# Optimization experiments

Measured on AMD Instinct MI355X. Metric: run time of the kernel, lower is better.

The kernel has to match this reference:

```python
import jax, jax.numpy as jnp
import numpy as np

D_AU, D_LM, D_GZ = 35, 196, 2   # au = 235 - 196 - 2 - 2
D, H = 128, 4
HD = D // H
LN_EPS = 1e-5


def setup_inputs() -> dict:
    key = jax.random.key(0)
    ks = jax.random.split(key, 12)
    s = lambda k, shape: jax.random.normal(k, shape, jnp.float32) * 0.02
    return {
        "video_feat": jax.random.normal(ks[0], (32, 4096, 235), jnp.float32),
        "au_w": s(ks[1], (D, D_AU)), "au_b": jnp.zeros((D,), jnp.float32),
        "lm_w": s(ks[2], (D, D_LM)), "lm_b": jnp.zeros((D,), jnp.float32),
        "gz_w": s(ks[3], (D, D_GZ)), "gz_b": jnp.zeros((D,), jnp.float32),
        "in_w": s(ks[4], (3 * D, D)), "in_b": jnp.zeros((3 * D,), jnp.float32),
        "out_w": s(ks[5], (D, D)), "out_b": jnp.zeros((D,), jnp.float32),
        "ln_g": jnp.ones((D,), jnp.float32), "ln_b": jnp.zeros((D,), jnp.float32),
        "w_w": s(ks[6], (1, D)), "w_b": jnp.zeros((1,), jnp.float32),
    }


def reference(video_feat, au_w, au_b, lm_w, lm_b, gz_w, gz_b,
              in_w, in_b, out_w, out_b, ln_g, ln_b, w_w, w_b):
    B, N, _ = video_feat.shape
    # split OpenFace3 features into semantic groups (meta dims unused, as in torch)
    au = video_feat[..., :D_AU]
    lm = video_feat[..., D_AU:D_AU + D_LM]
    gz = video_feat[..., D_AU + D_LM:D_AU + D_LM + D_GZ]
    au_h = au @ au_w.T + au_b
    lm_h = lm @ lm_w.T + lm_b
    gz_h = gz @ gz_w.T + gz_b
    tok = jnp.stack([au_h, lm_h, gz_h], axis=2).reshape(B * N, 3, D)  # (BN,3,D)

    # nn.MultiheadAttention (batch_first): packed in_proj then out_proj
    qkv = tok @ in_w.T + in_b                      # (BN,3,3D)
    q, k, v = jnp.split(qkv, 3, axis=-1)
    def heads(x):
        return x.reshape(-1, 3, H, HD).transpose(0, 2, 1, 3)  # (BN,H,3,HD)
    q, k, v = heads(q), heads(k), heads(v)
    scores = jnp.einsum('bhqd,bhkd->bhqk', q, k) / jnp.sqrt(jnp.float32(HD))
    attn = jax.nn.softmax(scores, axis=-1)
    o = jnp.einsum('bhqk,bhkd->bhqd', attn, v)
    o = o.transpose(0, 2, 1, 3).reshape(-1, 3, D)
    attn_out = o @ out_w.T + out_b

    # residual + LayerNorm
    x = attn_out + tok
    mu = x.mean(axis=-1, keepdims=True)
    var = x.var(axis=-1, keepdims=True)
    x = (x - mu) * jax.lax.rsqrt(var + LN_EPS) * ln_g + ln_b

    # softmax-weighted pooling over the 3 group tokens
    w = jax.nn.softmax((x @ w_w.T + w_b)[..., 0], axis=-1)  # (BN,3)
    fused = jnp.einsum('bt,btd->bd', w, x)
    return fused.reshape(B, N, D)
```

## Files before the change

### kernel.cpp

```cpp
#include <hip/hip_runtime.h>
#include <hip/hip_bf16.h>

typedef __hip_bfloat16 bf16;
typedef short  frag_t __attribute__((ext_vector_type(8)));
typedef float  f4     __attribute__((ext_vector_type(4)));
typedef unsigned short us8 __attribute__((ext_vector_type(8)));

#define NPOS (32 * 4096)
#define CIN  235

#define W1F 0
#define W2F 98304
#define W3F 147456
#define FRAG_TOTAL 163840
#define FP32_OFF_BYTES (FRAG_TOTAL * 2)
#define F_BIAS 0
#define F_INB  384
#define F_OUTB 768
#define F_LNG  896
#define F_LNB  1024
#define F_GW   1152
#define F_BW   1280
#define F_SGW  1281
#define WS2_BYTES (FP32_OFF_BYTES + 1282 * 4)

__device__ __forceinline__ float b2f(bf16 x) { return __bfloat162float(x); }
__device__ __forceinline__ unsigned short f2b(float v) {
    bf16 h = __float2bfloat16(v);
    return __builtin_bit_cast(unsigned short, h);
}
__device__ __forceinline__ float b2fr(unsigned short u) {
    return __bfloat162float(__builtin_bit_cast(bf16, u));
}
__device__ __forceinline__ bool probe_is_f32(const void* ln_g) {
    return *(const unsigned int*)ln_g == 0x3F800000u;
}
__device__ __forceinline__ float ldany(const void* p, int i, bool f32) {
    return f32 ? ((const float*)p)[i] : b2f(((const bf16*)p)[i]);
}
template<typename IT> __device__ __forceinline__ float ldv(const void* p, size_t i);
template<> __device__ __forceinline__ float ldv<float>(const void* p, size_t i) { return ((const float*)p)[i]; }
template<> __device__ __forceinline__ float ldv<bf16>(const void* p, size_t i)  { return b2f(((const bf16*)p)[i]); }
template<typename IT> __device__ __forceinline__ void stv(void* p, size_t i, float v);
template<> __device__ __forceinline__ void stv<float>(void* p, size_t i, float v) { ((float*)p)[i] = v; }
template<> __device__ __forceinline__ void stv<bf16>(void* p, size_t i, float v)  { ((bf16*)p)[i] = __float2bfloat16(v); }

__global__ __launch_bounds__(256) void kprep(
    const void* __restrict__ au_w, const void* __restrict__ au_b,
    const void* __restrict__ lm_w, const void* __restrict__ lm_b,
    const void* __restrict__ gz_w, const void* __restrict__ gz_b,
    const void* __restrict__ in_w, const void* __restrict__ in_b,
    const void* __restrict__ out_w, const void* __restrict__ out_b,
    const void* __restrict__ ln_g, const void* __restrict__ ln_b,
    const void* __restrict__ w_w, void* __restrict__ ws)
{
    const bool f32 = probe_is_f32(ln_g);
    int idx = blockIdx.x * 256 + threadIdx.x;
    unsigned short* wf = (unsigned short*)ws;
    float* wsf = (float*)((char*)ws + FP32_OFF_BYTES);

    if (idx < FRAG_TOTAL) {
        float val = 0.f;
        if (idx < W2F) {
            int r = idx, j = r & 7, lane = (r >> 3) & 63, q = r >> 9;
            int tn = q % 24, ks = q / 24;
            int k = ks * 32 + (lane >> 4) * 8 + j;
            int c = tn * 16 + (lane & 15);
            int t = c >> 7, jo = c & 127;
            if (t == 0 && k < 35)                   val = ldany(au_w, jo * 35 + k, f32);
            else if (t == 1 && k >= 35 && k < 231)  val = ldany(lm_w, jo * 196 + (k - 35), f32);
            else if (t == 2 && k >= 231 && k < 233) val = ldany(gz_w, jo * 2 + (k - 231), f32);
        } else if (idx < W3F) {
            int r = idx - W2F, j = r & 7, lane = (r >> 3) & 63, q = r >> 9;
            int tn = q % 24, ks = q / 24;
            int k = ks * 32 + (lane >> 4) * 8 + j;
            int c = tn * 16 + (lane & 15);
            val = ldany(in_w, c * 128 + k, f32);
        } else {
            int r = idx - W3F, j = r & 7, lane = (r >> 3) & 63, q = r >> 9;
            int tn = q & 7, ks = q >> 3;
            int k = ks * 32 + (lane >> 4) * 8 + j;
            int c = tn * 16 + (lane & 15);
            val = ldany(out_w, c * 128 + k, f32);
        }
        wf[idx] = f2b(val);
    } else if (idx < FRAG_TOTAL + 1280) {
        int i2 = idx - FRAG_TOTAL;
        float v;
        if (i2 < 384) {
            int t = i2 >> 7, jo = i2 & 127;
            const void* b = (t == 0) ? au_b : ((t == 1) ? lm_b : gz_b);
            v = ldany(b, jo, f32);
        } else if (i2 < 768)  v = ldany(in_b,  i2 - 384, f32);
        else if   (i2 < 896)  v = ldany(out_b, i2 - 768, f32);
        else if   (i2 < 1024) v = ldany(ln_g,  i2 - 896, f32);
        else if   (i2 < 1152) v = ldany(ln_b,  i2 - 1024, f32);
        else                  v = ldany(ln_g, i2 - 1152, f32) * ldany(w_w, i2 - 1152, f32);
        wsf[i2] = v;
    }
}

__global__ __launch_bounds__(64) void kscal(
    const void* __restrict__ ln_g, const void* __restrict__ ln_b,
    const void* __restrict__ w_w, const void* __restrict__ w_b,
    void* __restrict__ ws)
{
    const bool f32 = probe_is_f32(ln_g);
    float* wsf = (float*)((char*)ws + FP32_OFF_BYTES);
    int lane = threadIdx.x;
    float bw = 0.f, sg = 0.f;
    for (int j = lane; j < 128; j += 64) {
        float wwj = ldany(w_w, j, f32);
        bw += ldany(ln_b, j, f32) * wwj;
        sg += ldany(ln_g, j, f32) * wwj;
    }
#pragma unroll
    for (int off = 32; off >= 1; off >>= 1) {
        bw += __shfl_down(bw, off);
        sg += __shfl_down(sg, off);
    }
    if (lane == 0) {
        wsf[F_BW]  = bw + ldany(w_b, 0, f32);
        wsf[F_SGW] = sg;
    }
}

__global__ __launch_bounds__(256, 3) void sga_mfma(
    const void* __restrict__ vf, const void* __restrict__ ln_g,
    const void* __restrict__ ws, void* __restrict__ out)
{
    const bool f32 = probe_is_f32(ln_g);
    const int tid = threadIdx.x;
    const int w = tid >> 6, lane = tid & 63, quad = lane >> 4, l16 = lane & 15;
    const int p0 = blockIdx.x * 16;

    const frag_t* wfr = (const frag_t*)ws;
    const float*  wsf = (const float*)((const char*)ws + FP32_OFF_BYTES);

    __shared__ __align__(16) unsigned char u_buf[37632];
    __shared__ __align__(16) unsigned short s_tok[48][136];
    __shared__ float s_ar[576];
    __shared__ float s_mu[48], s_rs[48], s_w[16][3];

    unsigned short (*s_vf)[264]  = (unsigned short(*)[264])u_buf;
    unsigned short (*s_qkv)[392] = (unsigned short(*)[392])u_buf;
    float          (*s_x)[132]   = (float(*)[132])u_buf;

    for (int it = 0; it < 16; ++it) {
        int idx = it * 256 + tid;
        int row = idx >> 8, c = idx & 255;
        float v = 0.f;
        if (c < 233) {
            int gi = (p0 + row) * CIN + c;
            v = f32 ? ldv<float>(vf, gi) : ldv<bf16>(vf, gi);
        }
        s_vf[row][c] = f2b(v);
    }
    __syncthreads();

    {
        frag_t a[8];
#pragma unroll
        for (int ks = 0; ks < 8; ++ks)
            a[ks] = *(const frag_t*)&s_vf[l16][ks * 32 + quad * 8];
#pragma unroll
        for (int tn6 = 0; tn6 < 6; ++tn6) {
            int tn = w * 6 + tn6;
            f4 acc = {0.f, 0.f, 0.f, 0.f};
#pragma unroll
            for (int ks = 0; ks < 8; ++ks) {
                frag_t b = wfr[W1F / 8 + (ks * 24 + tn) * 64 + lane];
                acc = __builtin_amdgcn_mfma_f32_16x16x32_bf16(a[ks], b, acc, 0, 0, 0);
            }
            int c = tn * 16 + l16, t = c >> 7, jo = c & 127;
            float bias = wsf[F_BIAS + c];
#pragma unroll
            for (int r = 0; r < 4; ++r)
                s_tok[(quad * 4 + r) * 3 + t][jo] = f2b(acc[r] + bias);
        }
    }
    __syncthreads();

    {
        frag_t a[3][4];
#pragma unroll
        for (int rt = 0; rt < 3; ++rt)
#pragma unroll
            for (int ks = 0; ks < 4; ++ks)
                a[rt][ks] = *(const frag_t*)&s_tok[rt * 16 + l16][ks * 32 + quad * 8];
#pragma unroll
        for (int tn6 = 0; tn6 < 6; ++tn6) {
            int tn = w * 6 + tn6;
            f4 acc[3];
#pragma unroll
            for (int rt = 0; rt < 3; ++rt) acc[rt] = (f4){0.f, 0.f, 0.f, 0.f};
#pragma unroll
            for (int ks = 0; ks < 4; ++ks) {
                frag_t b = wfr[W2F / 8 + (ks * 24 + tn) * 64 + lane];
#pragma unroll
                for (int rt = 0; rt < 3; ++rt)
                    acc[rt] = __builtin_amdgcn_mfma_f32_16x16x32_bf16(a[rt][ks], b, acc[rt], 0, 0, 0);
            }
            int c = tn * 16 + l16;
            float bias = wsf[F_INB + c];
#pragma unroll
            for (int rt = 0; rt < 3; ++rt)
#pragma unroll
                for (int r = 0; r < 4; ++r)
                    s_qkv[rt * 16 + quad * 4 + r][c] = f2b(acc[rt][r] + bias);
        }
    }
    __syncthreads();

    if (tid < 192) {
        int p = tid / 12, r = tid % 12, h = r / 3, t = r % 3;
        const unsigned short* qrow = &s_qkv[p * 3 + t][h * 32];
        float sc0 = 0.f, sc1 = 0.f, sc2 = 0.f;
#pragma unroll
        for (int c4 = 0; c4 < 4; ++c4) {
            us8 qq = *(const us8*)&qrow[c4 * 8];
            float qf[8];
#pragma unroll
            for (int j = 0; j < 8; ++j) qf[j] = b2fr(qq[j]);
            us8 k0 = *(const us8*)&s_qkv[p * 3 + 0][128 + h * 32 + c4 * 8];
            us8 k1 = *(const us8*)&s_qkv[p * 3 + 1][128 + h * 32 + c4 * 8];
            us8 k2 = *(const us8*)&s_qkv[p * 3 + 2][128 + h * 32 + c4 * 8];
#pragma unroll
            for (int j = 0; j < 8; ++j) {
                sc0 += qf[j] * b2fr(k0[j]);
                sc1 += qf[j] * b2fr(k1[j]);
                sc2 += qf[j] * b2fr(k2[j]);
            }
        }
        const float scale = 0.17677669529663687f;
        sc0 *= scale; sc1 *= scale; sc2 *= scale;
        float m = fmaxf(sc0, fmaxf(sc1, sc2));
        float e0 = __expf(sc0 - m), e1 = __expf(sc1 - m), e2 = __expf(sc2 - m);
        float inv = 1.f / (e0 + e1 + e2);
        int base = ((p * 4 + h) * 3 + t) * 3;
        s_ar[base + 0] = e0 * inv;
        s_ar[base + 1] = e1 * inv;
        s_ar[base + 2] = e2 * inv;
    }
    __syncthreads();

    for (int u = 0; u < 3; ++u) {
        int unit = u * 256 + tid;
        int row = unit >> 4, c8 = (unit & 15) << 3;
        int p = row / 3, t = row - p * 3, h = c8 >> 5;
        int base = ((p * 4 + h) * 3 + t) * 3;
        float a0 = s_ar[base], a1 = s_ar[base + 1], a2 = s_ar[base + 2];
        us8 v0 = *(const us8*)&s_qkv[p * 3 + 0][256 + c8];
        us8 v1 = *(const us8*)&s_qkv[p * 3 + 1][256 + c8];
        us8 v2 = *(const us8*)&s_qkv[p * 3 + 2][256 + c8];
        us8 o;
#pragma unroll
        for (int jj = 0; jj < 8; ++jj)
            o[jj] = f2b(a0 * b2fr(v0[jj]) + a1 * b2fr(v1[jj]) + a2 * b2fr(v2[jj]));
        *(us8*)&s_qkv[row][c8] = o;
    }
    __syncthreads();

    frag_t of[3][4];
#pragma unroll
    for (int rt = 0; rt < 3; ++rt)
#pragma unroll
        for (int ks = 0; ks < 4; ++ks)
            of[rt][ks] = *(const frag_t*)&s_qkv[rt * 16 + l16][ks * 32 + quad * 8];
    __syncthreads();

    {
#pragma unroll
        for (int tn2 = 0; tn2 < 2; ++tn2) {
            int tn = w * 2 + tn2;
            f4 acc[3];
#pragma unroll
            for (int rt = 0; rt < 3; ++rt) acc[rt] = (f4){0.f, 0.f, 0.f, 0.f};
#pragma unroll
            for (int ks = 0; ks < 4; ++ks) {
                frag_t b = wfr[W3F / 8 + (ks * 8 + tn) * 64 + lane];
#pragma unroll
                for (int rt = 0; rt < 3; ++rt)
                    acc[rt] = __builtin_amdgcn_mfma_f32_16x16x32_bf16(of[rt][ks], b, acc[rt], 0, 0, 0);
            }
            int c = tn * 16 + l16;
            float ob = wsf[F_OUTB + c];
#pragma unroll
            for (int rt = 0; rt < 3; ++rt)
#pragma unroll
                for (int r = 0; r < 4; ++r) {
                    int row = rt * 16 + quad * 4 + r;
                    s_x[row][c] = acc[rt][r] + ob + b2fr(s_tok[row][c]);
                }
        }
    }
    __syncthreads();

    if (tid < 192) {
        int row = tid >> 2, part = tid & 3;
        float s = 0.f, ss = 0.f, sg = 0.f;
#pragma unroll
        for (int cc = 0; cc < 8; ++cc) {
            float4 xv = *(const float4*)&s_x[row][part * 32 + cc * 4];
            int cg = F_GW + part * 32 + cc * 4;
            s  += xv.x + xv.y + xv.z + xv.w;
            ss += xv.x * xv.x + xv.y * xv.y + xv.z * xv.z + xv.w * xv.w;
            sg += xv.x * wsf[cg] + xv.y * wsf[cg + 1] + xv.z * wsf[cg + 2] + xv.w * wsf[cg + 3];
        }
        int b = (row * 4 + part) * 3;
        s_ar[b] = s; s_ar[b + 1] = ss; s_ar[b + 2] = sg;
    }
    __syncthreads();
    if (tid < 64) {
        float lg = 0.f;
        if (lane < 48) {
            float s = 0.f, ss = 0.f, sg = 0.f;
#pragma unroll
            for (int part = 0; part < 4; ++part) {
                int b = (lane * 4 + part) * 3;
                s += s_ar[b]; ss += s_ar[b + 1]; sg += s_ar[b + 2];
            }
            float mu  = s * (1.f / 128.f);
            float var = ss * (1.f / 128.f) - mu * mu;
            float rs  = rsqrtf(var + 1e-5f);
            s_mu[lane] = mu; s_rs[lane] = rs;
            lg = wsf[F_BW] + rs * (sg - mu * wsf[F_SGW]);
        }
        float l0 = __shfl(lg, 3 * lane);
        float l1 = __shfl(lg, 3 * lane + 1);
        float l2 = __shfl(lg, 3 * lane + 2);
        if (lane < 16) {
            float m = fmaxf(l0, fmaxf(l1, l2));
            float e0 = __expf(l0 - m), e1 = __expf(l1 - m), e2 = __expf(l2 - m);
            float inv = 1.f / (e0 + e1 + e2);
            s_w[lane][0] = e0 * inv; s_w[lane][1] = e1 * inv; s_w[lane][2] = e2 * inv;
        }
    }
    __syncthreads();

    {
        int j = tid & 127;
        float g = wsf[F_LNG + j], b = wsf[F_LNB + j];
#pragma unroll
        for (int it = 0; it < 8; ++it) {
            int p = it * 2 + (tid >> 7);
            float f = 0.f;
#pragma unroll
            for (int t = 0; t < 3; ++t) {
                int row = p * 3 + t;
                f += s_w[p][t] * ((s_x[row][j] - s_mu[row]) * s_rs[row] * g + b);
            }
            size_t oidx = (size_t)(p0 + p) * 128 + j;
            if (f32) stv<float>(out, oidx, f); else stv<bf16>(out, oidx, f);
        }
    }
}

#define P 4
struct SmemFB {
    float vf[P][233];
    alignas(16) float tok[P][128][4];
    float qkv[P][3][384];
    float att[P][4][3][3];
    alignas(16) float o[P][128][4];
    float x[P][3][128];
    float red[P][3][2];
    float w[P][4];
};

template<typename IT>
__device__ void sga_fb_body(SmemFB& s,
    const void* vf, const void* au_w, const void* au_b, const void* lm_w,
    const void* lm_b, const void* gz_w, const void* gz_b, const void* in_w,
    const void* in_b, const void* out_w, const void* out_b, const void* ln_g,
    const void* ln_b, const void* w_w, const void* w_b, void* out)
{
    const int j = threadIdx.x;
    const int p0 = blockIdx.x * P;
    for (int p = 0; p < P; ++p) {
        size_t rb = (size_t)(p0 + p) * CIN;
        for (int d = j; d < 233; d += 128) s.vf[p][d] = ldv<IT>(vf, rb + d);
    }
    __syncthreads();
    {
        float a_au[P], a_lm[P], a_gz[P];
        const float bau = ldv<IT>(au_b, j), blm = ldv<IT>(lm_b, j), bgz = ldv<IT>(gz_b, j);
#pragma unroll
        for (int p = 0; p < P; ++p) { a_au[p] = bau; a_lm[p] = blm; a_gz[p] = bgz; }
        for (int d = 0; d < 35; ++d) {
            float w = ldv<IT>(au_w, j * 35 + d);
#pragma unroll
            for (int p = 0; p < P; ++p) a_au[p] += s.vf[p][d] * w;
        }
        for (int d = 0; d < 196; ++d) {
            float w = ldv<IT>(lm_w, j * 196 + d);
#pragma unroll
            for (int p = 0; p < P; ++p) a_lm[p] += s.vf[p][35 + d] * w;
        }
        for (int d = 0; d < 2; ++d) {
            float w = ldv<IT>(gz_w, j * 2 + d);
#pragma unroll
            for (int p = 0; p < P; ++p) a_gz[p] += s.vf[p][231 + d] * w;
        }
#pragma unroll
        for (int p = 0; p < P; ++p) {
            s.tok[p][j][0] = a_au[p]; s.tok[p][j][1] = a_lm[p];
            s.tok[p][j][2] = a_gz[p]; s.tok[p][j][3] = 0.f;
        }
    }
    __syncthreads();
    {
        float acc[P][3][3];
#pragma unroll
        for (int rr = 0; rr < 3; ++rr) {
            float b = ldv<IT>(in_b, j + rr * 128);
#pragma unroll
            for (int p = 0; p < P; ++p)
#pragma unroll
                for (int t = 0; t < 3; ++t) acc[p][rr][t] = b;
        }
        for (int d = 0; d < 128; ++d) {
            const float w0 = ldv<IT>(in_w, (j)       * 128 + d);
            const float w1 = ldv<IT>(in_w, (j + 128) * 128 + d);
            const float w2 = ldv<IT>(in_w, (j + 256) * 128 + d);
#pragma unroll
            for (int p = 0; p < P; ++p) {
                const float4 tv = *(const float4*)&s.tok[p][d][0];
                acc[p][0][0] += tv.x * w0; acc[p][0][1] += tv.y * w0; acc[p][0][2] += tv.z * w0;
                acc[p][1][0] += tv.x * w1; acc[p][1][1] += tv.y * w1; acc[p][1][2] += tv.z * w1;
                acc[p][2][0] += tv.x * w2; acc[p][2][1] += tv.y * w2; acc[p][2][2] += tv.z * w2;
            }
        }
#pragma unroll
        for (int p = 0; p < P; ++p)
#pragma unroll
            for (int rr = 0; rr < 3; ++rr)
#pragma unroll
                for (int t = 0; t < 3; ++t)
                    s.qkv[p][t][j + rr * 128] = acc[p][rr][t];
    }
    __syncthreads();
    for (int i = j; i < P * 36; i += 128) {
        int p = i / 36, r = i % 36, h = r / 9, t = (r / 3) % 3, k = r % 3;
        const float* qp = &s.qkv[p][t][h * 32];
        const float* kp = &s.qkv[p][k][128 + h * 32];
        float sc = 0.f;
#pragma unroll
        for (int d = 0; d < 32; ++d) sc += qp[d] * kp[d];
        s.att[p][h][t][k] = sc * 0.17677669529663687f;
    }
    __syncthreads();
    if (j < P * 12) {
        int p = j / 12, r = j % 12, h = r / 3, t = r % 3;
        float l0 = s.att[p][h][t][0], l1 = s.att[p][h][t][1], l2 = s.att[p][h][t][2];
        float m = fmaxf(l0, fmaxf(l1, l2));
        float e0 = __expf(l0 - m), e1 = __expf(l1 - m), e2 = __expf(l2 - m);
        float inv = 1.f / (e0 + e1 + e2);
        s.att[p][h][t][0] = e0 * inv; s.att[p][h][t][1] = e1 * inv; s.att[p][h][t][2] = e2 * inv;
    }
    __syncthreads();
    {
        const int h = j >> 5;
#pragma unroll
        for (int p = 0; p < P; ++p) {
            const float v0 = s.qkv[p][0][256 + j];
            const float v1 = s.qkv[p][1][256 + j];
            const float v2 = s.qkv[p][2][256 + j];
#pragma unroll
            for (int t = 0; t < 3; ++t)
                s.o[p][j][t] = s.att[p][h][t][0] * v0 + s.att[p][h][t][1] * v1
                             + s.att[p][h][t][2] * v2;
            s.o[p][j][3] = 0.f;
        }
    }
    __syncthreads();
    {
        float acc[P][3];
        const float ob = ldv<IT>(out_b, j);
#pragma unroll
        for (int p = 0; p < P; ++p)
#pragma unroll
            for (int t = 0; t < 3; ++t) acc[p][t] = ob;
        for (int d = 0; d < 128; ++d) {
            const float w = ldv<IT>(out_w, j * 128 + d);
#pragma unroll
            for (int p = 0; p < P; ++p) {
                const float4 ov = *(const float4*)&s.o[p][d][0];
                acc[p][0] += ov.x * w; acc[p][1] += ov.y * w; acc[p][2] += ov.z * w;
            }
        }
#pragma unroll
        for (int p = 0; p < P; ++p)
#pragma unroll
            for (int t = 0; t < 3; ++t)
                s.x[p][t][j] = acc[p][t] + s.tok[p][j][t];
    }
    __syncthreads();
    if (j < P * 3) {
        int p = j / 3, t = j % 3;
        float sm = 0.f, ss = 0.f;
        for (int d = 0; d < 128; ++d) { float v = s.x[p][t][d]; sm += v; ss += v * v; }
        float mu = sm * (1.f / 128.f);
        float var = ss * (1.f / 128.f) - mu * mu;
        s.red[p][t][0] = mu; s.red[p][t][1] = rsqrtf(var + 1e-5f);
    }
    __syncthreads();
    {
        const float g = ldv<IT>(ln_g, j), b = ldv<IT>(ln_b, j);
#pragma unroll
        for (int p = 0; p < P; ++p)
#pragma unroll
            for (int t = 0; t < 3; ++t) {
                float mu = s.red[p][t][0], rs = s.red[p][t][1];
                s.x[p][t][j] = (s.x[p][t][j] - mu) * rs * g + b;
            }
    }
    __syncthreads();
    if (j < P * 3) {
        int p = j / 3, t = j % 3;
        float lg = ldv<IT>(w_b, 0);
        for (int d = 0; d < 128; ++d) lg += s.x[p][t][d] * ldv<IT>(w_w, d);
        s.red[p][t][0] = lg;
    }
    __syncthreads();
    if (j < P) {
        float l0 = s.red[j][0][0], l1 = s.red[j][1][0], l2 = s.red[j][2][0];
        float m = fmaxf(l0, fmaxf(l1, l2));
        float e0 = __expf(l0 - m), e1 = __expf(l1 - m), e2 = __expf(l2 - m);
        float inv = 1.f / (e0 + e1 + e2);
        s.w[j][0] = e0 * inv; s.w[j][1] = e1 * inv; s.w[j][2] = e2 * inv;
    }
    __syncthreads();
#pragma unroll
    for (int p = 0; p < P; ++p) {
        float f = s.w[p][0] * s.x[p][0][j] + s.w[p][1] * s.x[p][1][j]
                + s.w[p][2] * s.x[p][2][j];
        stv<IT>(out, (size_t)(p0 + p) * 128 + j, f);
    }
}

__global__ __launch_bounds__(128) void sga_fb(
    const void* vf, const void* au_w, const void* au_b, const void* lm_w,
    const void* lm_b, const void* gz_w, const void* gz_b, const void* in_w,
    const void* in_b, const void* out_w, const void* out_b, const void* ln_g,
    const void* ln_b, const void* w_w, const void* w_b, void* out)
{
    __shared__ SmemFB s;
    if (probe_is_f32(ln_g))
        sga_fb_body<float>(s, vf, au_w, au_b, lm_w, lm_b, gz_w, gz_b, in_w, in_b,
                           out_w, out_b, ln_g, ln_b, w_w, w_b, out);
    else
        sga_fb_body<bf16>(s, vf, au_w, au_b, lm_w, lm_b, gz_w, gz_b, in_w, in_b,
                          out_w, out_b, ln_g, ln_b, w_w, w_b, out);
}

extern "C" void kernel_launch(void* const* d_in, const int* in_sizes, int n_in,
                              void* d_out, int out_size, void* d_ws, size_t ws_size,
                              hipStream_t stream) {
    const void* vf    = d_in[0];
    const void* au_w  = d_in[1];
    const void* au_b  = d_in[2];
    const void* lm_w  = d_in[3];
    const void* lm_b  = d_in[4];
    const void* gz_w  = d_in[5];
    const void* gz_b  = d_in[6];
    const void* in_w  = d_in[7];
    const void* in_b  = d_in[8];
    const void* out_w = d_in[9];
    const void* out_b = d_in[10];
    const void* ln_g  = d_in[11];
    const void* ln_b  = d_in[12];
    const void* w_w   = d_in[13];
    const void* w_b   = d_in[14];

    if (ws_size >= (size_t)WS2_BYTES) {
        kprep<<<645, 256, 0, stream>>>(au_w, au_b, lm_w, lm_b, gz_w, gz_b,
                                       in_w, in_b, out_w, out_b, ln_g, ln_b,
                                       w_w, d_ws);
        kscal<<<1, 64, 0, stream>>>(ln_g, ln_b, w_w, w_b, d_ws);
        sga_mfma<<<NPOS / 16, 256, 0, stream>>>(vf, ln_g, d_ws, d_out);
    } else {
        sga_fb<<<NPOS / P, 128, 0, stream>>>(vf, au_w, au_b, lm_w, lm_b, gz_w,
                                             gz_b, in_w, in_b, out_w, out_b,
                                             ln_g, ln_b, w_w, w_b, d_out);
    }
}
```

Measured before the change: 411.7 us.

## Shrink shared memory, vectorize loads/stores, MFMA attention scores, fold kscal into kprep

Cuts the main kernel's shared memory by splitting the QKV projection into a Q/K pass and a separate V pass that reuses the buffer, and XOR-swizzles the token tile. Together with launch bounds raised from 3 to 4 blocks, this aims for higher occupancy. Input rows are loaded with float4/us8 vector loads, attention scores use MFMA instead of scalar dot products, and the final pooling is vectorized with a folded LayerNorm form. The kscal kernel is merged into kprep as an extra block to save a launch. The split adds a barrier and a second pass over the token fragments, and many unrelated changes are bundled.

Result: faster. 356.2 us (-13.5%).

```diff
diff --git a/kernel.cpp b/kernel.cpp
--- a/kernel.cpp
+++ b/kernel.cpp
@@ -5,6 +5,7 @@
 typedef short  frag_t __attribute__((ext_vector_type(8)));
 typedef float  f4     __attribute__((ext_vector_type(4)));
 typedef unsigned short us8 __attribute__((ext_vector_type(8)));
+typedef unsigned short us4 __attribute__((ext_vector_type(4)));
 
 #define NPOS (32 * 4096)
 #define CIN  235
@@ -45,6 +46,10 @@
 template<> __device__ __forceinline__ void stv<float>(void* p, size_t i, float v) { ((float*)p)[i] = v; }
 template<> __device__ __forceinline__ void stv<bf16>(void* p, size_t i, float v)  { ((bf16*)p)[i] = __float2bfloat16(v); }
 
+__device__ __forceinline__ int tok_idx(int row, int col) {
+    return row * 128 + (col ^ ((row & 7) << 3));
+}
+
 __global__ __launch_bounds__(256) void kprep(
     const void* __restrict__ au_w, const void* __restrict__ au_b,
     const void* __restrict__ lm_w, const void* __restrict__ lm_b,
@@ -52,13 +57,36 @@
     const void* __restrict__ in_w, const void* __restrict__ in_b,
     const void* __restrict__ out_w, const void* __restrict__ out_b,
     const void* __restrict__ ln_g, const void* __restrict__ ln_b,
-    const void* __restrict__ w_w, void* __restrict__ ws)
+    const void* __restrict__ w_w, const void* __restrict__ w_b,
+    void* __restrict__ ws)
 {
     const bool f32 = probe_is_f32(ln_g);
-    int idx = blockIdx.x * 256 + threadIdx.x;
     unsigned short* wf = (unsigned short*)ws;
     float* wsf = (float*)((char*)ws + FP32_OFF_BYTES);
 
+    if (blockIdx.x == 645) {
+        if (threadIdx.x < 64) {
+            int lane = threadIdx.x;
+            float bw = 0.f, sg = 0.f;
+            for (int j = lane; j < 128; j += 64) {
+                float wwj = ldany(w_w, j, f32);
+                bw += ldany(ln_b, j, f32) * wwj;
+                sg += ldany(ln_g, j, f32) * wwj;
+            }
+#pragma unroll
+            for (int off = 32; off >= 1; off >>= 1) {
+                bw += __shfl_down(bw, off);
+                sg += __shfl_down(sg, off);
+            }
+            if (lane == 0) {
+                wsf[F_BW]  = bw + ldany(w_b, 0, f32);
+                wsf[F_SGW] = sg;
+            }
+        }
+        return;
+    }
+
+    int idx = blockIdx.x * 256 + threadIdx.x;
     if (idx < FRAG_TOTAL) {
         float val = 0.f;
         if (idx < W2F) {
@@ -100,32 +128,7 @@
     }
 }
 
-__global__ __launch_bounds__(64) void kscal(
-    const void* __restrict__ ln_g, const void* __restrict__ ln_b,
-    const void* __restrict__ w_w, const void* __restrict__ w_b,
-    void* __restrict__ ws)
-{
-    const bool f32 = probe_is_f32(ln_g);
-    float* wsf = (float*)((char*)ws + FP32_OFF_BYTES);
-    int lane = threadIdx.x;
-    float bw = 0.f, sg = 0.f;
-    for (int j = lane; j < 128; j += 64) {
-        float wwj = ldany(w_w, j, f32);
-        bw += ldany(ln_b, j, f32) * wwj;
-        sg += ldany(ln_g, j, f32) * wwj;
-    }
-#pragma unroll
-    for (int off = 32; off >= 1; off >>= 1) {
-        bw += __shfl_down(bw, off);
-        sg += __shfl_down(sg, off);
-    }
-    if (lane == 0) {
-        wsf[F_BW]  = bw + ldany(w_b, 0, f32);
-        wsf[F_SGW] = sg;
-    }
-}
-
-__global__ __launch_bounds__(256, 3) void sga_mfma(
+__global__ __launch_bounds__(256, 4) void sga_mfma(
     const void* __restrict__ vf, const void* __restrict__ ln_g,
     const void* __restrict__ ws, void* __restrict__ out)
 {
@@ -137,24 +140,53 @@
     const frag_t* wfr = (const frag_t*)ws;
     const float*  wsf = (const float*)((const char*)ws + FP32_OFF_BYTES);
 
-    __shared__ __align__(16) unsigned char u_buf[37632];
-    __shared__ __align__(16) unsigned short s_tok[48][136];
+    __shared__ __align__(16) unsigned char u_buf[25344];
+    __shared__ __align__(16) unsigned short s_tok[6144];
     __shared__ float s_ar[576];
     __shared__ float s_mu[48], s_rs[48], s_w[16][3];
 
-    unsigned short (*s_vf)[264]  = (unsigned short(*)[264])u_buf;
-    unsigned short (*s_qkv)[392] = (unsigned short(*)[392])u_buf;
-    float          (*s_x)[132]   = (float(*)[132])u_buf;
-
-    for (int it = 0; it < 16; ++it) {
-        int idx = it * 256 + tid;
-        int row = idx >> 8, c = idx & 255;
-        float v = 0.f;
-        if (c < 233) {
-            int gi = (p0 + row) * CIN + c;
-            v = f32 ? ldv<float>(vf, gi) : ldv<bf16>(vf, gi);
-        }
-        s_vf[row][c] = f2b(v);
+    unsigned short (*s_vf)[264] = (unsigned short(*)[264])u_buf;
+    unsigned short (*s_qk)[264] = (unsigned short(*)[264])u_buf;
+    float          (*s_x)[132]  = (float(*)[132])u_buf;
+
+    for (int z = tid; z < 384; z += 256) {
+        int rz = z / 24, cz = z - rz * 24;
+        s_vf[rz][233 + cz] = 0;
+    }
+    if (f32) {
+        const float* src = (const float*)vf + (size_t)p0 * CIN;
+#pragma unroll
+        for (int it = 0; it < 4; ++it) {
+            int idx = it * 256 + tid;
+            if (idx < 940) {
+                float4 vv = *(const float4*)(src + idx * 4);
+                int e = idx * 4;
+                int r = e / 235, c = e - r * 235;
+#pragma unroll
+                for (int j = 0; j < 4; ++j) {
+                    int rj = r, cj = c + j;
+                    if (cj >= 235) { rj++; cj -= 235; }
+                    if (cj < 233) s_vf[rj][cj] = f2b(((const float*)&vv)[j]);
+                }
+            }
+        }
+    } else {
+        const unsigned short* src = (const unsigned short*)vf + (size_t)p0 * CIN;
+#pragma unroll
+        for (int it = 0; it < 2; ++it) {
+            int idx = it * 256 + tid;
+            if (idx < 470) {
+                us8 vv = *(const us8*)(src + idx * 8);
+                int e = idx * 8;
+                int r = e / 235, c = e - r * 235;
+#pragma unroll
+                for (int j = 0; j < 8; ++j) {
+                    int rj = r, cj = c + j;
+                    if (cj >= 235) { rj++; cj -= 235; }
+                    if (cj < 233) s_vf[rj][cj] = vv[j];
+                }
+            }
+        }
     }
     __syncthreads();
 
@@ -176,7 +208,7 @@
             float bias = wsf[F_BIAS + c];
 #pragma unroll
             for (int r = 0; r < 4; ++r)
-                s_tok[(quad * 4 + r) * 3 + t][jo] = f2b(acc[r] + bias);
+                s_tok[tok_idx((quad * 4 + r) * 3 + t, jo)] = f2b(acc[r] + bias);
         }
     }
     __syncthreads();
@@ -187,10 +219,10 @@
         for (int rt = 0; rt < 3; ++rt)
 #pragma unroll
             for (int ks = 0; ks < 4; ++ks)
-                a[rt][ks] = *(const frag_t*)&s_tok[rt * 16 + l16][ks * 32 + quad * 8];
-#pragma unroll
-        for (int tn6 = 0; tn6 < 6; ++tn6) {
-            int tn = w * 6 + tn6;
+                a[rt][ks] = *(const frag_t*)&s_tok[tok_idx(rt * 16 + l16, ks * 32 + quad * 8)];
+#pragma unroll
+        for (int tn4 = 0; tn4 < 4; ++tn4) {
+            int tn = w * 4 + tn4;
             f4 acc[3];
 #pragma unroll
             for (int rt = 0; rt < 3; ++rt) acc[rt] = (f4){0.f, 0.f, 0.f, 0.f};
@@ -207,40 +239,78 @@
             for (int rt = 0; rt < 3; ++rt)
 #pragma unroll
                 for (int r = 0; r < 4; ++r)
-                    s_qkv[rt * 16 + quad * 4 + r][c] = f2b(acc[rt][r] + bias);
-        }
-    }
-    __syncthreads();
-
-    if (tid < 192) {
-        int p = tid / 12, r = tid % 12, h = r / 3, t = r % 3;
-        const unsigned short* qrow = &s_qkv[p * 3 + t][h * 32];
-        float sc0 = 0.f, sc1 = 0.f, sc2 = 0.f;
-#pragma unroll
-        for (int c4 = 0; c4 < 4; ++c4) {
-            us8 qq = *(const us8*)&qrow[c4 * 8];
-            float qf[8];
-#pragma unroll
-            for (int j = 0; j < 8; ++j) qf[j] = b2fr(qq[j]);
-            us8 k0 = *(const us8*)&s_qkv[p * 3 + 0][128 + h * 32 + c4 * 8];
-            us8 k1 = *(const us8*)&s_qkv[p * 3 + 1][128 + h * 32 + c4 * 8];
-            us8 k2 = *(const us8*)&s_qkv[p * 3 + 2][128 + h * 32 + c4 * 8];
-#pragma unroll
-            for (int j = 0; j < 8; ++j) {
-                sc0 += qf[j] * b2fr(k0[j]);
-                sc1 += qf[j] * b2fr(k1[j]);
-                sc2 += qf[j] * b2fr(k2[j]);
-            }
-        }
-        const float scale = 0.17677669529663687f;
-        sc0 *= scale; sc1 *= scale; sc2 *= scale;
-        float m = fmaxf(sc0, fmaxf(sc1, sc2));
-        float e0 = __expf(sc0 - m), e1 = __expf(sc1 - m), e2 = __expf(sc2 - m);
-        float inv = 1.f / (e0 + e1 + e2);
-        int base = ((p * 4 + h) * 3 + t) * 3;
-        s_ar[base + 0] = e0 * inv;
-        s_ar[base + 1] = e1 * inv;
-        s_ar[base + 2] = e2 * inv;
+                    s_qk[rt * 16 + quad * 4 + r][c] = f2b(acc[rt][r] + bias);
+        }
+    }
+    __syncthreads();
+
+    {
+        const int h = w;
+        frag_t qf[3], kf[3];
+#pragma unroll
+        for (int t = 0; t < 3; ++t) {
+            qf[t] = *(const frag_t*)&s_qk[l16 * 3 + t][h * 32 + quad * 8];
+            kf[t] = *(const frag_t*)&s_qk[l16 * 3 + t][128 + h * 32 + quad * 8];
+        }
+        float dv[3][3];
+        const int rr = l16 & 3;
+#pragma unroll
+        for (int t = 0; t < 3; ++t)
+#pragma unroll
+            for (int k = 0; k < 3; ++k) {
+                f4 acc = {0.f, 0.f, 0.f, 0.f};
+                acc = __builtin_amdgcn_mfma_f32_16x16x32_bf16(qf[t], kf[k], acc, 0, 0, 0);
+                float d = acc[0];
+                d = rr == 1 ? acc[1] : d;
+                d = rr == 2 ? acc[2] : d;
+                d = rr == 3 ? acc[3] : d;
+                dv[t][k] = d;
+            }
+        if ((l16 >> 2) == quad) {
+            const float scale = 0.17677669529663687f;
+            int base0 = (l16 * 4 + h) * 9;
+#pragma unroll
+            for (int t = 0; t < 3; ++t) {
+                float s0 = dv[t][0] * scale, s1 = dv[t][1] * scale, s2 = dv[t][2] * scale;
+                float m = fmaxf(s0, fmaxf(s1, s2));
+                float e0 = __expf(s0 - m), e1 = __expf(s1 - m), e2 = __expf(s2 - m);
+                float inv = 1.f / (e0 + e1 + e2);
+                s_ar[base0 + t * 3 + 0] = e0 * inv;
+                s_ar[base0 + t * 3 + 1] = e1 * inv;
+                s_ar[base0 + t * 3 + 2] = e2 * inv;
+            }
+        }
+    }
+    __syncthreads();
+
+    {
+        frag_t a[3][4];
+#pragma unroll
+        for (int rt = 0; rt < 3; ++rt)
+#pragma unroll
+            for (int ks = 0; ks < 4; ++ks)
+                a[rt][ks] = *(const frag_t*)&s_tok[tok_idx(rt * 16 + l16, ks * 32 + quad * 8)];
+#pragma unroll
+        for (int tn2 = 0; tn2 < 2; ++tn2) {
+            int tn = 16 + w * 2 + tn2;
+            f4 acc[3];
+#pragma unroll
+            for (int rt = 0; rt < 3; ++rt) acc[rt] = (f4){0.f, 0.f, 0.f, 0.f};
+#pragma unroll
+            for (int ks = 0; ks < 4; ++ks) {
+                frag_t b = wfr[W2F / 8 + (ks * 24 + tn) * 64 + lane];
+#pragma unroll
+                for (int rt = 0; rt < 3; ++rt)
+                    acc[rt] = __builtin_amdgcn_mfma_f32_16x16x32_bf16(a[rt][ks], b, acc[rt], 0, 0, 0);
+            }
+            int c = tn * 16 + l16;
+            float bias = wsf[F_INB + c];
+#pragma unroll
+            for (int rt = 0; rt < 3; ++rt)
+#pragma unroll
+                for (int r = 0; r < 4; ++r)
+                    s_qk[rt * 16 + quad * 4 + r][c - 256] = f2b(acc[rt][r] + bias);
+        }
     }
     __syncthreads();
 
@@ -248,16 +318,16 @@
         int unit = u * 256 + tid;
         int row = unit >> 4, c8 = (unit & 15) << 3;
         int p = row / 3, t = row - p * 3, h = c8 >> 5;
-        int base = ((p * 4 + h) * 3 + t) * 3;
+        int base = (p * 4 + h) * 9 + t * 3;
         float a0 = s_ar[base], a1 = s_ar[base + 1], a2 = s_ar[base + 2];
-        us8 v0 = *(const us8*)&s_qkv[p * 3 + 0][256 + c8];
-        us8 v1 = *(const us8*)&s_qkv[p * 3 + 1][256 + c8];
-        us8 v2 = *(const us8*)&s_qkv[p * 3 + 2][256 + c8];
+        us8 v0 = *(const us8*)&s_qk[p * 3 + 0][c8];
+        us8 v1 = *(const us8*)&s_qk[p * 3 + 1][c8];
+        us8 v2 = *(const us8*)&s_qk[p * 3 + 2][c8];
         us8 o;
 #pragma unroll
         for (int jj = 0; jj < 8; ++jj)
             o[jj] = f2b(a0 * b2fr(v0[jj]) + a1 * b2fr(v1[jj]) + a2 * b2fr(v2[jj]));
-        *(us8*)&s_qkv[row][c8] = o;
+        *(us8*)&s_qk[row][128 + c8] = o;
     }
     __syncthreads();
 
@@ -266,7 +336,7 @@
     for (int rt = 0; rt < 3; ++rt)
 #pragma unroll
         for (int ks = 0; ks < 4; ++ks)
-            of[rt][ks] = *(const frag_t*)&s_qkv[rt * 16 + l16][ks * 32 + quad * 8];
+            of[rt][ks] = *(const frag_t*)&s_qk[rt * 16 + l16][128 + ks * 32 + quad * 8];
     __syncthreads();
 
     {
@@ -290,7 +360,7 @@
 #pragma unroll
                 for (int r = 0; r < 4; ++r) {
                     int row = rt * 16 + quad * 4 + r;
-                    s_x[row][c] = acc[rt][r] + ob + b2fr(s_tok[row][c]);
+                    s_x[row][c] = acc[rt][r] + ob + b2fr(s_tok[tok_idx(row, c)]);
                 }
         }
     }
@@ -339,19 +409,33 @@
     __syncthreads();
 
     {
-        int j = tid & 127;
-        float g = wsf[F_LNG + j], b = wsf[F_LNB + j];
-#pragma unroll
-        for (int it = 0; it < 8; ++it) {
-            int p = it * 2 + (tid >> 7);
-            float f = 0.f;
-#pragma unroll
-            for (int t = 0; t < 3; ++t) {
-                int row = p * 3 + t;
-                f += s_w[p][t] * ((s_x[row][j] - s_mu[row]) * s_rs[row] * g + b);
-            }
-            size_t oidx = (size_t)(p0 + p) * 128 + j;
-            if (f32) stv<float>(out, oidx, f); else stv<bf16>(out, oidx, f);
+#pragma unroll
+        for (int it = 0; it < 2; ++it) {
+            int task = it * 256 + tid;
+            int p = task >> 5, cg = (task & 31) * 4;
+            int row0 = p * 3;
+            float c0 = s_w[p][0] * s_rs[row0];
+            float c1 = s_w[p][1] * s_rs[row0 + 1];
+            float c2 = s_w[p][2] * s_rs[row0 + 2];
+            float C  = c0 * s_mu[row0] + c1 * s_mu[row0 + 1] + c2 * s_mu[row0 + 2];
+            float4 g = *(const float4*)&wsf[F_LNG + cg];
+            float4 b = *(const float4*)&wsf[F_LNB + cg];
+            float4 x0 = *(const float4*)&s_x[row0][cg];
+            float4 x1 = *(const float4*)&s_x[row0 + 1][cg];
+            float4 x2 = *(const float4*)&s_x[row0 + 2][cg];
+            float4 f;
+            f.x = (c0 * x0.x + c1 * x1.x + c2 * x2.x - C) * g.x + b.x;
+            f.y = (c0 * x0.y + c1 * x1.y + c2 * x2.y - C) * g.y + b.y;
+            f.z = (c0 * x0.z + c1 * x1.z + c2 * x2.z - C) * g.z + b.z;
+            f.w = (c0 * x0.w + c1 * x1.w + c2 * x2.w - C) * g.w + b.w;
+            size_t o0 = (size_t)(p0 + p) * 128 + cg;
+            if (f32) {
+                *(float4*)((float*)out + o0) = f;
+            } else {
+                us4 pv;
+                pv[0] = f2b(f.x); pv[1] = f2b(f.y); pv[2] = f2b(f.z); pv[3] = f2b(f.w);
+                *(us4*)((bf16*)out + o0) = pv;
+            }
         }
     }
 }
@@ -574,10 +658,9 @@
     const void* w_b   = d_in[14];
 
     if (ws_size >= (size_t)WS2_BYTES) {
-        kprep<<<645, 256, 0, stream>>>(au_w, au_b, lm_w, lm_b, gz_w, gz_b,
+        kprep<<<646, 256, 0, stream>>>(au_w, au_b, lm_w, lm_b, gz_w, gz_b,
                                        in_w, in_b, out_w, out_b, ln_g, ln_b,
-                                       w_w, d_ws);
-        kscal<<<1, 64, 0, stream>>>(ln_g, ln_b, w_w, w_b, d_ws);
+                                       w_w, w_b, d_ws);
         sga_mfma<<<NPOS / 16, 256, 0, stream>>>(vf, ln_g, d_ws, d_out);
     } else {
         sga_fb<<<NPOS / P, 128, 0, stream>>>(vf, au_w, au_b, lm_w, lm_b, gz_w,
```
